# Optimization experiments

Hardware: AMD Instinct MI355X
Metric: run time of the kernel (lower is better)

Reference implementation:

```python
import jax, jax.numpy as jnp
import numpy as np

EPS = 1e-5
H = 128          # hidden_size
IN = 75          # input_size
T = 128          # seq len == window_size
B = 1024
OUT = 256        # lstm_output_size


def _bn(x, gamma, beta):
    # training-mode batch norm over the batch dim (biased variance, as in PyTorch BN)
    m = x.mean(axis=0)
    v = x.var(axis=0)
    return gamma * (x - m) * jax.lax.rsqrt(v + EPS) + beta


def _run_bnlstm_layer(xs, Wih, Whh, b, gih, bih, ghh, bhh, gc, bc):
    # xs: (T, B, D). Returns hidden stream (T, B, H).
    Bsz = xs.shape[1]
    h0 = jnp.zeros((Bsz, H), xs.dtype)
    c0 = jnp.zeros((Bsz, H), xs.dtype)

    def step(carry, x):
        h, c = carry
        gates = _bn(x @ Wih, gih, bih) + _bn(h @ Whh, ghh, bhh) + b  # (B, 4H)
        f, i, o, g = jnp.split(gates, 4, axis=1)                     # gate order f,i,o,g
        c1 = jax.nn.sigmoid(f) * c + jax.nn.sigmoid(i) * jnp.tanh(g)
        h1 = jax.nn.sigmoid(o) * jnp.tanh(_bn(c1, gc, bc))
        return (h1, c1), h1

    (_, _), hs = jax.lax.scan(step, (h0, c0), xs)
    return hs


def setup_inputs() -> dict:
    key = jax.random.key(0)
    ks = jax.random.split(key, 12)
    s = 0.05
    d = {
        'sequences': jax.random.normal(ks[0], (B, T, IN), jnp.float32),
        # layer 0 BNLSTM cell params (weights stored as (in, 4H) so y = x @ W)
        'Wih0': jax.random.normal(ks[1], (IN, 4 * H), jnp.float32) * s,
        'Whh0': jax.random.normal(ks[2], (H, 4 * H), jnp.float32) * s,
        'b0': jnp.zeros((4 * H,), jnp.float32),
        'gih0': jnp.full((4 * H,), 0.1, jnp.float32),
        'bih0': jnp.zeros((4 * H,), jnp.float32),
        'ghh0': jnp.full((4 * H,), 0.1, jnp.float32),
        'bhh0': jnp.zeros((4 * H,), jnp.float32),
        'gc0': jnp.full((H,), 0.1, jnp.float32),
        'bc0': jnp.zeros((H,), jnp.float32),
        # layer 1
        'Wih1': jax.random.normal(ks[3], (H, 4 * H), jnp.float32) * s,
        'Whh1': jax.random.normal(ks[4], (H, 4 * H), jnp.float32) * s,
        'b1': jnp.zeros((4 * H,), jnp.float32),
        'gih1': jnp.full((4 * H,), 0.1, jnp.float32),
        'bih1': jnp.zeros((4 * H,), jnp.float32),
        'ghh1': jnp.full((4 * H,), 0.1, jnp.float32),
        'bhh1': jnp.zeros((4 * H,), jnp.float32),
        'gc1': jnp.full((H,), 0.1, jnp.float32),
        'bc1': jnp.zeros((H,), jnp.float32),
        # fc: hidden -> lstm_output_size; decoder: lstm_output_size -> T*IN
        'fc_w': jax.random.normal(ks[5], (H, OUT), jnp.float32) * s,
        'fc_b': jnp.zeros((OUT,), jnp.float32),
        'dec_w': jax.random.normal(ks[6], (OUT, T * IN), jnp.float32) * s,
        'dec_b': jnp.zeros((T * IN,), jnp.float32),
    }
    return d


def reference(sequences, Wih0, Whh0, b0, gih0, bih0, ghh0, bhh0, gc0, bc0,
              Wih1, Whh1, b1, gih1, bih1, ghh1, bhh1, gc1, bc1,
              fc_w, fc_b, dec_w, dec_b):
    xs = jnp.transpose(sequences, (1, 0, 2))  # (T, B, IN), time-major
    hs0 = _run_bnlstm_layer(xs, Wih0, Whh0, b0, gih0, bih0, ghh0, bhh0, gc0, bc0)
    hs1 = _run_bnlstm_layer(hs0, Wih1, Whh1, b1, gih1, bih1, ghh1, bhh1, gc1, bc1)
    last = hs1[-1]                       # (B, H): last time step of top layer
    emb = last @ fc_w + fc_b             # (B, OUT)
    out = emb @ dec_w + dec_b            # (B, T*IN)
    return out.reshape(-1, T, IN)
```

## Files before the change

kernel.cpp:

```cpp
#include <hip/hip_runtime.h>
#include <stdint.h>
#include <stddef.h>

#define TT   128
#define BB   1024
#define INN  75
#define HH   128
#define KXP  96
#define OUTN 256
#define DECN 9600
#define EPSB 1e-5f
#define NRB  16
#define RWS  64

typedef short v8s __attribute__((ext_vector_type(8)));
typedef float v4f __attribute__((ext_vector_type(4)));
typedef unsigned short ush;
typedef unsigned int   u32;
typedef unsigned long long u64;

#define MFMA(A,B,C) __builtin_amdgcn_mfma_f32_16x16x32_bf16((A),(B),(C),0,0,0)

__device__ __align__(256) ush g_xpad[(size_t)TT * BB * KXP];
__device__ __align__(256) u64 g_G1[(size_t)TT * 32 * BB * 4];
__device__ __align__(256) ush g_wtih0[512 * KXP];
__device__ __align__(256) ush g_wthh0[512 * HH];
__device__ __align__(256) ush g_wtih1[512 * HH];
__device__ __align__(256) ush g_wthh1[512 * HH];
__device__ __align__(256) ush g_fcwt[OUTN * HH];
__device__ __align__(256) ush g_decwt[(size_t)DECN * OUTN];
__device__ __align__(256) ush g_emb[BB * OUTN];
__device__ __align__(256) u64 g_hfin[BB * 32];

__device__ __align__(256) u64 g_th0[(size_t)TT * BB * 64];
__device__ __align__(256) u64 g_gp[(size_t)2 * TT * 2 * NRB * 512];
__device__ __align__(256) u64 g_cp[(size_t)2 * TT * 2 * NRB * 64];
__device__ __align__(256) u64 g_soc[(size_t)2 * TT * 2 * BB * 64];
__device__ u32 g_ep[64];

__device__ __forceinline__ ush f2bf(float f) {
  u32 u = __float_as_uint(f);
  u32 r = (u + 0x7FFFu + ((u >> 16) & 1u)) >> 16;
  return (ush)r;
}
__device__ __forceinline__ float bf2f(ush u) { return __uint_as_float(((u32)u) << 16); }
__device__ __forceinline__ float sigf(float x)  { return 1.f / (1.f + __expf(-x)); }
__device__ __forceinline__ float tanhf_(float x){ float e = __expf(2.f * x); return 1.f - 2.f / (e + 1.f); }
__device__ __forceinline__ v8s ld8(const ush* p) { return *reinterpret_cast<const v8s*>(p); }
__device__ __forceinline__ int origcol(int m) { return (m & 3) * 128 + (m >> 4) * 4 + ((m >> 2) & 3); }

__device__ __forceinline__ u64 ald(const u64* p) {
  return __hip_atomic_load(p, __ATOMIC_RELAXED, __HIP_MEMORY_SCOPE_AGENT);
}
__device__ __forceinline__ void ast(u64* p, u64 v) {
  __hip_atomic_store(p, v, __ATOMIC_RELAXED, __HIP_MEMORY_SCOPE_AGENT);
}
__device__ __forceinline__ u64 pk24(u32 tag, float a, float b) {
  return ((u64)(tag & 0xFFFFu) << 48)
       | ((u64)(__float_as_uint(a) >> 8) << 24)
       | (u64)(__float_as_uint(b) >> 8);
}
__device__ __forceinline__ float upA24(u64 w) { return __uint_as_float(((u32)(w >> 24) & 0xFFFFFFu) << 8); }
__device__ __forceinline__ float upB24(u64 w) { return __uint_as_float(((u32)w & 0xFFFFFFu) << 8); }
__device__ __forceinline__ u32 tg16(u64 w) { return (u32)(w >> 48); }
__device__ __forceinline__ int hswz(int r, int b) { return (r * 256 + b) ^ ((r & 7) << 4); }
__device__ __forceinline__ v8s ld8l(const char* lds, int r, int b) {
  return *reinterpret_cast<const v8s*>(lds + hswz(r, b));
}

__global__ void kpackx(const float* __restrict__ seq) {
  int idx = blockIdx.x * 256 + threadIdx.x;
  int kk = idx % KXP; int rest = idx / KXP;
  int b = rest % BB;  int t = rest / BB;
  float v = (kk < INN) ? seq[((size_t)b * TT + t) * INN + kk] : 0.f;
  g_xpad[idx] = f2bf(v);
}

__global__ void kpackw(const float* __restrict__ Wih0, const float* __restrict__ Whh0,
                       const float* __restrict__ Wih1, const float* __restrict__ Whh1,
                       const float* __restrict__ fcw,  const float* __restrict__ decw) {
  int idx = blockIdx.x * 256 + threadIdx.x;
  if (idx < 49152) {
    int m = idx / KXP, k = idx % KXP;
    g_wtih0[idx] = f2bf((k < INN) ? Wih0[k * 512 + origcol(m)] : 0.f);
  } else if (idx < 114688) {
    int j = idx - 49152; int m = j / HH, k = j % HH;
    g_wthh0[j] = f2bf(Whh0[k * 512 + origcol(m)]);
  } else if (idx < 180224) {
    int j = idx - 114688; int m = j / HH, k = j % HH;
    g_wtih1[j] = f2bf(Wih1[k * 512 + origcol(m)]);
  } else if (idx < 245760) {
    int j = idx - 180224; int m = j / HH, k = j % HH;
    g_wthh1[j] = f2bf(Whh1[k * 512 + origcol(m)]);
  } else if (idx < 278528) {
    int j = idx - 245760; int c = j / HH, k = j % HH;
    g_fcwt[j] = f2bf(fcw[k * OUTN + c]);
  } else {
    int j = idx - 278528; int n = j % DECN, k = j / DECN;
    g_decwt[(size_t)n * OUTN + k] = f2bf(decw[(size_t)k * DECN + n]);
  }
}

__global__ __launch_bounds__(512) void kprep(const float* __restrict__ gih0,
                                             const float* __restrict__ bih0,
                                             const float* __restrict__ b0) {
  const int t = blockIdx.x >> 3, ct = blockIdx.x & 7;
  const int tid = threadIdx.x, wv = tid >> 6, l = tid & 63;
  const int lm = l & 15, lq = l >> 4;
  const int R0 = wv * 128;
  __shared__ float sred[8][64][2];
  __shared__ float scoef[64][2];

  v8s af[4][3];
#pragma unroll
  for (int tt = 0; tt < 4; ++tt)
#pragma unroll
    for (int ks = 0; ks < 3; ++ks)
      af[tt][ks] = ld8(&g_wtih0[(ct * 64 + tt * 16 + lm) * KXP + ks * 32 + lq * 8]);

  const v4f vz = {0.f, 0.f, 0.f, 0.f};
  v4f acc[8][4];
#pragma unroll
  for (int mt = 0; mt < 8; ++mt)
#pragma unroll
    for (int tt = 0; tt < 4; ++tt) acc[mt][tt] = vz;

#pragma unroll
  for (int mt = 0; mt < 8; ++mt) {
    const ush* xr = g_xpad + ((size_t)t * BB + R0 + mt * 16 + lm) * KXP + lq * 8;
    v8s bx0 = ld8(xr), bx1 = ld8(xr + 32), bx2 = ld8(xr + 64);
#pragma unroll
    for (int tt = 0; tt < 4; ++tt) {
      acc[mt][tt] = MFMA(af[tt][0], bx0, acc[mt][tt]);
      acc[mt][tt] = MFMA(af[tt][1], bx1, acc[mt][tt]);
      acc[mt][tt] = MFMA(af[tt][2], bx2, acc[mt][tt]);
    }
  }
  float S[4][4], Q[4][4];
#pragma unroll
  for (int tt = 0; tt < 4; ++tt)
#pragma unroll
    for (int r = 0; r < 4; ++r) {
      float s = 0.f, q = 0.f;
#pragma unroll
      for (int mt = 0; mt < 8; ++mt) { float a = acc[mt][tt][r]; s += a; q += a * a; }
#pragma unroll
      for (int off = 1; off < 16; off <<= 1) { s += __shfl_xor(s, off); q += __shfl_xor(q, off); }
      S[tt][r] = s; Q[tt][r] = q;
    }
  if (lm == 0)
#pragma unroll
    for (int tt = 0; tt < 4; ++tt)
#pragma unroll
      for (int r = 0; r < 4; ++r) {
        sred[wv][tt * 16 + lq * 4 + r][0] = S[tt][r];
        sred[wv][tt * 16 + lq * 4 + r][1] = Q[tt][r];
      }
  __syncthreads();
  if (tid < 64) {
    float Sa = 0.f, Qa = 0.f;
#pragma unroll
    for (int w8 = 0; w8 < 8; ++w8) { Sa += sred[w8][tid][0]; Qa += sred[w8][tid][1]; }
    int oc = origcol(ct * 64 + tid);
    float m_ = Sa * (1.f / BB), v_ = Qa * (1.f / BB) - m_ * m_;
    float A = gih0[oc] * rsqrtf(v_ + EPSB);
    scoef[tid][0] = A; scoef[tid][1] = bih0[oc] - A * m_ + b0[oc];
  }
  __syncthreads();
  float CA[4][4], CD[4][4];
#pragma unroll
  for (int tt = 0; tt < 4; ++tt)
#pragma unroll
    for (int r = 0; r < 4; ++r) {
      CA[tt][r] = scoef[tt * 16 + lq * 4 + r][0];
      CD[tt][r] = scoef[tt * 16 + lq * 4 + r][1];
    }
#pragma unroll
  for (int mt = 0; mt < 8; ++mt) {
    const int row = R0 + mt * 16 + lm;
#pragma unroll
    for (int tt = 0; tt < 4; ++tt) {
      const int g = ct * 4 + tt;
      u32 lo = (u32)f2bf(CA[tt][0] * acc[mt][tt][0] + CD[tt][0])
             | ((u32)f2bf(CA[tt][1] * acc[mt][tt][1] + CD[tt][1]) << 16);
      u32 hi = (u32)f2bf(CA[tt][2] * acc[mt][tt][2] + CD[tt][2])
             | ((u32)f2bf(CA[tt][3] * acc[mt][tt][3] + CD[tt][3]) << 16);
      g_G1[(((size_t)t * 32 + g) * BB + row) * 4 + lq] = (u64)lo | ((u64)hi << 32);
    }
  }
}

__global__ __launch_bounds__(512, 1) void krec7(
    const float* __restrict__ ghh0, const float* __restrict__ bhh0,
    const float* __restrict__ gc0,  const float* __restrict__ bc0,
    const float* __restrict__ gih1, const float* __restrict__ bih1,
    const float* __restrict__ ghh1, const float* __restrict__ bhh1,
    const float* __restrict__ b1,   const float* __restrict__ gc1,
    const float* __restrict__ bc1) {
  const int bid = blockIdx.x;
  const int L = bid >> 5, H = (bid >> 4) & 1, rb = bid & 15;
  const int tid = threadIdx.x, w = tid >> 6, l = tid & 63;
  const int lm = l & 15, lq = l >> 4;
  const int R0 = rb * RWS;

  __shared__ u64 s_hA_[2048];
  __shared__ u64 s_hB_[2048];
  __shared__ float s_gA[256], s_gB[256], s_bs[256];
  __shared__ float s_cgM[128], s_cbM[128];
  __shared__ float s_cA[256], s_cB[256], s_cD[256], s_mual[2][256];
  __shared__ float s_ccA[128], s_ccD[128];
  __shared__ u32 s_base;
  char* const hA = reinterpret_cast<char*>(s_hA_);
  char* const hB = reinterpret_cast<char*>(s_hB_);

  if (tid == 0)
    s_base = __hip_atomic_load(&g_ep[bid], __ATOMIC_RELAXED, __HIP_MEMORY_SCOPE_AGENT);
  if (tid < 256) {
    const int oc = origcol(H * 256 + tid);
    if (L == 0) { s_gA[tid] = ghh0[oc]; s_gB[tid] = 0.f; s_bs[tid] = bhh0[oc]; }
    else { s_gA[tid] = gih1[oc]; s_gB[tid] = ghh1[oc];
           s_bs[tid] = bih1[oc] + bhh1[oc] + b1[oc]; }
  }
  if (tid < 128) {
    s_cgM[tid] = (L ? gc1 : gc0)[tid];
    s_cbM[tid] = (L ? bc1 : bc0)[tid];
  }
  __syncthreads();
  const u32 base = s_base;

  v8s afA[2][4], afB[2][4];
  {
    const ush* wA = L ? g_wtih1 : g_wthh0;
#pragma unroll
    for (int ct = 0; ct < 2; ++ct)
#pragma unroll
      for (int ks = 0; ks < 4; ++ks) {
        const int mrow = H * 256 + (w * 2 + ct) * 16 + lm;
        afA[ct][ks] = ld8(&wA[mrow * HH + ks * 32 + lq * 8]);
        if (L) afB[ct][ks] = ld8(&g_wthh1[mrow * HH + ks * 32 + lq * 8]);
      }
  }

  float creg[4][2] = {{0.f,0.f},{0.f,0.f},{0.f,0.f},{0.f,0.f}};
  const v4f vz = {0.f, 0.f, 0.f, 0.f};

#pragma unroll 1
  for (int t = 0; t < TT; ++t) {
    const u32 tagF = base + (u32)t + 1;
    const u32 t16 = tagF & 0xFFFFu;
    v4f PA[4][2], PB[4][2];
#pragma unroll
    for (int mt = 0; mt < 4; ++mt) {
      PA[mt][0] = vz; PA[mt][1] = vz; PB[mt][0] = vz; PB[mt][1] = vz;
    }
    u64 g1v[4][2];

    if (L == 0) {
#pragma unroll
      for (int mt = 0; mt < 4; ++mt)
#pragma unroll
        for (int ct = 0; ct < 2; ++ct)
          g1v[mt][ct] = g_G1[(((size_t)t * 32 + H * 16 + w * 2 + ct) * BB
                              + R0 + mt * 16 + lm) * 4 + lq];
    } else {
      const int row = tid >> 3, j0 = (tid & 7) * 8;
      const u64* p = g_th0 + ((size_t)t * BB + R0 + row) * 64 + j0;
      u64 v[8];
#pragma unroll
      for (int k = 0; k < 8; ++k) v[k] = ald(p + k);
      for (;;) {
        bool ok = true;
#pragma unroll
        for (int k = 0; k < 8; ++k)
          if ((u32)(v[k] >> 32) != tagF) { v[k] = ald(p + k); ok = false; }
        if (ok) break;
        __builtin_amdgcn_s_sleep(1);
      }
#pragma unroll
      for (int k = 0; k < 8; ++k)
        *reinterpret_cast<u32*>(hA + hswz(row, (j0 + k) * 4)) = (u32)v[k];
    }
    __syncthreads();

    if (L == 0) {
      if (t > 0) {
#pragma unroll
        for (int mt = 0; mt < 4; ++mt)
#pragma unroll
          for (int ks = 0; ks < 4; ++ks) {
            const v8s f = ld8l(hA, mt * 16 + lm, ks * 64 + lq * 16);
            PA[mt][0] = MFMA(afA[0][ks], f, PA[mt][0]);
            PA[mt][1] = MFMA(afA[1][ks], f, PA[mt][1]);
          }
      }
    } else {
#pragma unroll
      for (int mt = 0; mt < 4; ++mt)
#pragma unroll
        for (int ks = 0; ks < 4; ++ks) {
          const v8s f = ld8l(hA, mt * 16 + lm, ks * 64 + lq * 16);
          PA[mt][0] = MFMA(afA[0][ks], f, PA[mt][0]);
          PA[mt][1] = MFMA(afA[1][ks], f, PA[mt][1]);
        }
      if (t > 0) {
#pragma unroll
        for (int mt = 0; mt < 4; ++mt)
#pragma unroll
          for (int ks = 0; ks < 4; ++ks) {
            const v8s f = ld8l(hB, mt * 16 + lm, ks * 64 + lq * 16);
            PB[mt][0] = MFMA(afB[0][ks], f, PB[mt][0]);
            PB[mt][1] = MFMA(afB[1][ks], f, PB[mt][1]);
          }
      }
    }

    u64* const gpO = g_gp + ((((size_t)L * TT + t) * 2 + H) * NRB + rb) * 512;
#pragma unroll
    for (int ct = 0; ct < 2; ++ct) {
      float sA[4], qA[4], sB[4], qB[4];
#pragma unroll
      for (int r = 0; r < 4; ++r) {
        float s1 = PA[0][ct][r] + PA[1][ct][r] + PA[2][ct][r] + PA[3][ct][r];
        float q1 = PA[0][ct][r]*PA[0][ct][r] + PA[1][ct][r]*PA[1][ct][r]
                 + PA[2][ct][r]*PA[2][ct][r] + PA[3][ct][r]*PA[3][ct][r];
        float s2 = PB[0][ct][r] + PB[1][ct][r] + PB[2][ct][r] + PB[3][ct][r];
        float q2 = PB[0][ct][r]*PB[0][ct][r] + PB[1][ct][r]*PB[1][ct][r]
                 + PB[2][ct][r]*PB[2][ct][r] + PB[3][ct][r]*PB[3][ct][r];
#pragma unroll
        for (int off = 1; off < 16; off <<= 1) {
          s1 += __shfl_xor(s1, off); q1 += __shfl_xor(q1, off);
          if (L) { s2 += __shfl_xor(s2, off); q2 += __shfl_xor(q2, off); }
        }
        sA[r] = s1; qA[r] = q1; sB[r] = s2; qB[r] = q2;
      }
      if (lm == 0) {
        const int m0 = (w * 2 + ct) * 16 + lq * 4;
#pragma unroll
        for (int r = 0; r < 4; ++r) {
          ast(&gpO[(m0 + r) * 2], pk24(tagF, sA[r], qA[r]));
          if (L) ast(&gpO[(m0 + r) * 2 + 1], pk24(tagF, sB[r], qB[r]));
        }
      }
    }
    __syncthreads();

    {
      const int st = tid >> 8, m = tid & 255;
      if (st == 0 || L == 1) {
        const u64* pb = g_gp + (((size_t)L * TT + t) * 2 + H) * NRB * 512 + m * 2 + st;
        u64 v[16];
#pragma unroll
        for (int r2 = 0; r2 < 16; ++r2) v[r2] = ald(pb + (size_t)r2 * 512);
        for (;;) {
          bool ok = true;
#pragma unroll
          for (int r2 = 0; r2 < 16; ++r2)
            if (tg16(v[r2]) != t16) { v[r2] = ald(pb + (size_t)r2 * 512); ok = false; }
          if (ok) break;
          __builtin_amdgcn_s_sleep(1);
        }
        float S = 0.f, Q = 0.f;
#pragma unroll
        for (int r2 = 0; r2 < 16; ++r2) { S += upA24(v[r2]); Q += upB24(v[r2]); }
        const float mu = S * (1.f / BB), var = Q * (1.f / BB) - mu * mu;
        const float A = (st ? s_gB[m] : s_gA[m]) * rsqrtf(var + EPSB);
        if (st == 0) s_cA[m] = A; else s_cB[m] = A;
        s_mual[st][m] = A * mu;
      }
    }
    __syncthreads();
    if (tid < 256) s_cD[tid] = s_bs[tid] - s_mual[0][tid] - (L ? s_mual[1][tid] : 0.f);
    __syncthreads();

    u64* const cpO = g_cp + ((((size_t)L * TT + t) * 2 + H) * NRB + rb) * 64;
    u64* const socO = g_soc + (((size_t)L * TT + t) * 2 + H) * BB * 64;
    float soq[4][2], cq_[4][2];
#pragma unroll
    for (int ct = 0; ct < 2; ++ct) {
      const int mb = (w * 2 + ct) * 16 + lq * 4;
      const v4f cA = *reinterpret_cast<const v4f*>(&s_cA[mb]);
      const v4f cD = *reinterpret_cast<const v4f*>(&s_cD[mb]);
      const v4f cB = *reinterpret_cast<const v4f*>(&s_cB[mb]);
      const int ul = (w * 2 + ct) * 4 + lq;
      float cs = 0.f, cqs = 0.f;
#pragma unroll
      for (int mt = 0; mt < 4; ++mt) {
        float gv[4];
        if (L == 0) {
          const u64 g1 = g1v[mt][ct];
          gv[0] = bf2f((ush)g1)         + cA[0] * PA[mt][ct][0] + cD[0];
          gv[1] = bf2f((ush)(g1 >> 16)) + cA[1] * PA[mt][ct][1] + cD[1];
          gv[2] = bf2f((ush)(g1 >> 32)) + cA[2] * PA[mt][ct][2] + cD[2];
          gv[3] = bf2f((ush)(g1 >> 48)) + cA[3] * PA[mt][ct][3] + cD[3];
        } else {
#pragma unroll
          for (int r = 0; r < 4; ++r)
            gv[r] = cA[r] * PA[mt][ct][r] + cB[r] * PB[mt][ct][r] + cD[r];
        }
        const float cold = (t == 0) ? 0.f : creg[mt][ct];
        const float c1 = sigf(gv[0]) * cold + sigf(gv[1]) * tanhf_(gv[3]);
        creg[mt][ct] = c1;
        const float so = sigf(gv[2]);
        const u64 ws = pk24(tagF, so, c1);
        ast(&socO[(size_t)(R0 + mt * 16 + lm) * 64 + ul], ws);
        const float soQ = upA24(ws), cQ = upB24(ws);
        soq[mt][ct] = soQ; cq_[mt][ct] = cQ;
        cs += cQ; cqs += cQ * cQ;
      }
#pragma unroll
      for (int off = 1; off < 16; off <<= 1) { cs += __shfl_xor(cs, off); cqs += __shfl_xor(cqs, off); }
      if (lm == 0) ast(&cpO[ul], pk24(tagF, cs, cqs));
    }
    __syncthreads();

    u64 sv[8];
    if (tid < 128) {
      const int Hs = tid >> 6, us = tid & 63;
      const u64* pc = g_cp + (((size_t)L * TT + t) * 2 + Hs) * NRB * 64 + us;
      u64 v[16];
#pragma unroll
      for (int r2 = 0; r2 < 16; ++r2) v[r2] = ald(pc + (size_t)r2 * 64);
      for (;;) {
        bool ok = true;
#pragma unroll
        for (int r2 = 0; r2 < 16; ++r2)
          if (tg16(v[r2]) != t16) { v[r2] = ald(pc + (size_t)r2 * 64); ok = false; }
        if (ok) break;
        __builtin_amdgcn_s_sleep(1);
      }
      float S = 0.f, Q = 0.f;
#pragma unroll
      for (int r2 = 0; r2 < 16; ++r2) { S += upA24(v[r2]); Q += upB24(v[r2]); }
      const float mu = S * (1.f / BB), var = Q * (1.f / BB) - mu * mu;
      const float ac = s_cgM[tid] * rsqrtf(var + EPSB);
      s_ccA[tid] = ac; s_ccD[tid] = s_cbM[tid] - ac * mu;
    }
    {
      const int rloc = tid >> 3, u0 = (tid & 7) * 8;
      const u64* ps = g_soc + (((size_t)L * TT + t) * 2 + (1 - H)) * BB * 64
                    + (size_t)(R0 + rloc) * 64 + u0;
#pragma unroll
      for (int k = 0; k < 8; ++k) sv[k] = ald(ps + k);
      for (;;) {
        bool ok = true;
#pragma unroll
        for (int k = 0; k < 8; ++k)
          if (tg16(sv[k]) != t16) { sv[k] = ald(ps + k); ok = false; }
        if (ok) break;
        __builtin_amdgcn_s_sleep(1);
      }
    }
    __syncthreads();

    char* const town = L ? hB : hA;
#pragma unroll
    for (int ct = 0; ct < 2; ++ct) {
      const int ul = (w * 2 + ct) * 4 + lq;
      const int ug = H * 64 + ul;
      const float ac = s_ccA[ug], dc = s_ccD[ug];
#pragma unroll
      for (int mt = 0; mt < 4; ++mt) {
        const int rowl = mt * 16 + lm;
        const u32 v = (u32)f2bf(soq[mt][ct] * tanhf_(ac * cq_[mt][ct] + dc));
        const u32 a = v | (__shfl_xor(v, 16) << 16);
        if (lq == 0 || lq == 2) {
          const int jg = H * 32 + (w * 2 + ct) * 2 + (lq >> 1);
          *reinterpret_cast<u32*>(town + hswz(rowl, jg * 4)) = a;
          if (L == 0)
            ast(&g_th0[((size_t)t * BB + R0 + rowl) * 64 + jg], (((u64)tagF) << 32) | a);
        }
        if (L == 1 && t == TT - 1) {
          const u32 b2 = __shfl_xor(a, 32);
          if (lq == 0)
            g_hfin[(size_t)(R0 + rowl) * 32 + H * 16 + (w * 2 + ct)] = (u64)a | ((u64)b2 << 32);
        }
      }
    }
    {
      const int rloc = tid >> 3, u0 = (tid & 7) * 8;
#pragma unroll
      for (int k = 0; k < 8; ++k) {
        const int ugs = (1 - H) * 64 + u0 + k;
        const float hs = upA24(sv[k]) * tanhf_(s_ccA[ugs] * upB24(sv[k]) + s_ccD[ugs]);
        *reinterpret_cast<ush*>(town + hswz(rloc, ugs * 2)) = f2bf(hs);
      }
    }
    __syncthreads();
  }

  if (tid == 0)
    __hip_atomic_store(&g_ep[bid], base + TT, __ATOMIC_RELAXED, __HIP_MEMORY_SCOPE_AGENT);
}

__global__ __launch_bounds__(256) void kfc(const float* __restrict__ fcb) {
  const int tid = threadIdx.x, w = tid >> 6, l = tid & 63;
  const int lm = l & 15, lq = l >> 4;
  const int col = blockIdx.x * 16 + lm;
  const ush* hsrc = reinterpret_cast<const ush*>(g_hfin);
  v8s bf[4];
#pragma unroll
  for (int ks = 0; ks < 4; ++ks) bf[ks] = ld8(&g_fcwt[col * HH + ks * 32 + lq * 8]);
  const float bias = fcb[col];
  const v4f vz = {0.f, 0.f, 0.f, 0.f};
#pragma unroll
  for (int mt = 0; mt < 16; ++mt) {
    const int rowa = w * 256 + mt * 16 + lm;
    const ush* ap = hsrc + (size_t)rowa * HH + lq * 8;
    v4f acc = vz;
#pragma unroll
    for (int ks = 0; ks < 4; ++ks)
      acc = MFMA(ld8(ap + ks * 32), bf[ks], acc);
#pragma unroll
    for (int r = 0; r < 4; ++r) {
      int row = w * 256 + mt * 16 + lq * 4 + r;
      g_emb[row * OUTN + col] = f2bf(acc[r] + bias);
    }
  }
}

__global__ __launch_bounds__(256) void kdec(const float* __restrict__ decb, float* __restrict__ out) {
  const int tid = threadIdx.x, wv = tid >> 6, l = tid & 63;
  const int lm = l & 15, lq = l >> 4;
  const int c0 = blockIdx.x * 16;
  const int R0 = wv * 256;
  v8s af[8];
#pragma unroll
  for (int ks = 0; ks < 8; ++ks) af[ks] = ld8(&g_decwt[(size_t)(c0 + lm) * OUTN + ks * 32 + lq * 8]);
  float bias[4];
#pragma unroll
  for (int r = 0; r < 4; ++r) bias[r] = decb[c0 + lq * 4 + r];
  const v4f vz = {0.f, 0.f, 0.f, 0.f};
#pragma unroll
  for (int mt = 0; mt < 16; ++mt) {
    const int row = R0 + mt * 16 + lm;
    const ush* bp = g_emb + (size_t)row * OUTN + lq * 8;
    v4f acc = vz;
#pragma unroll
    for (int ks = 0; ks < 8; ++ks)
      acc = MFMA(af[ks], ld8(bp + ks * 32), acc);
    v4f o;
#pragma unroll
    for (int r = 0; r < 4; ++r) o[r] = acc[r] + bias[r];
    *reinterpret_cast<v4f*>(&out[(size_t)row * DECN + c0 + lq * 4]) = o;
  }
}

extern "C" void kernel_launch(void* const* d_in, const int* in_sizes, int n_in,
                              void* d_out, int out_size, void* d_ws, size_t ws_size,
                              hipStream_t stream) {
  const float* seq  = (const float*)d_in[0];
  const float* Wih0 = (const float*)d_in[1];
  const float* Whh0 = (const float*)d_in[2];
  const float* b0   = (const float*)d_in[3];
  const float* gih0 = (const float*)d_in[4];
  const float* bih0 = (const float*)d_in[5];
  const float* ghh0 = (const float*)d_in[6];
  const float* bhh0 = (const float*)d_in[7];
  const float* gc0  = (const float*)d_in[8];
  const float* bc0  = (const float*)d_in[9];
  const float* Wih1 = (const float*)d_in[10];
  const float* Whh1 = (const float*)d_in[11];
  const float* b1   = (const float*)d_in[12];
  const float* gih1 = (const float*)d_in[13];
  const float* bih1 = (const float*)d_in[14];
  const float* ghh1 = (const float*)d_in[15];
  const float* bhh1 = (const float*)d_in[16];
  const float* gc1  = (const float*)d_in[17];
  const float* bc1  = (const float*)d_in[18];
  const float* fcw  = (const float*)d_in[19];
  const float* fcb  = (const float*)d_in[20];
  const float* decw = (const float*)d_in[21];
  const float* decb = (const float*)d_in[22];
  float* out = (float*)d_out;
  (void)in_sizes; (void)n_in; (void)out_size; (void)d_ws; (void)ws_size;

  kpackx<<<dim3((TT * BB * KXP) / 256), dim3(256), 0, stream>>>(seq);
  kpackw<<<dim3(10688), dim3(256), 0, stream>>>(Wih0, Whh0, Wih1, Whh1, fcw, decw);
  kprep<<<dim3(TT * 8), dim3(512), 0, stream>>>(gih0, bih0, b0);
  krec7<<<dim3(64), dim3(512), 0, stream>>>(ghh0, bhh0, gc0, bc0,
                                            gih1, bih1, ghh1, bhh1, b1, gc1, bc1);
  kfc<<<dim3(16), dim3(256), 0, stream>>>(fcb);
  kdec<<<dim3(600), dim3(256), 0, stream>>>(decb, out);
}
```

Before: 3.038 ms.

## Use 4-slot ring buffers for cross-block exchange with layer-1 backpressure flags

```diff
diff --git a/kernel.cpp b/kernel.cpp
--- a/kernel.cpp
+++ b/kernel.cpp
@@ -32,10 +32,11 @@
 __device__ __align__(256) ush g_emb[BB * OUTN];
 __device__ __align__(256) u64 g_hfin[BB * 32];
 
-__device__ __align__(256) u64 g_th0[(size_t)TT * BB * 64];
-__device__ __align__(256) u64 g_gp[(size_t)2 * TT * 2 * NRB * 512];
-__device__ __align__(256) u64 g_cp[(size_t)2 * TT * 2 * NRB * 64];
-__device__ __align__(256) u64 g_soc[(size_t)2 * TT * 2 * BB * 64];
+__device__ __align__(256) u64 g_th0[4][BB * 64];
+__device__ __align__(256) u64 g_gp[2][2][4][NRB * 512];
+__device__ __align__(256) u64 g_cp[2][4][2][NRB * 64];
+__device__ __align__(256) u64 g_soc[2][4][2][BB * 64];
+__device__ u32 g_l1p[2][NRB * 32];
 __device__ u32 g_ep[64];
 
 __device__ __forceinline__ ush f2bf(float f) {
@@ -53,6 +54,12 @@
   return __hip_atomic_load(p, __ATOMIC_RELAXED, __HIP_MEMORY_SCOPE_AGENT);
 }
 __device__ __forceinline__ void ast(u64* p, u64 v) {
+  __hip_atomic_store(p, v, __ATOMIC_RELAXED, __HIP_MEMORY_SCOPE_AGENT);
+}
+__device__ __forceinline__ u32 ald32(const u32* p) {
+  return __hip_atomic_load(p, __ATOMIC_RELAXED, __HIP_MEMORY_SCOPE_AGENT);
+}
+__device__ __forceinline__ void ast32(u32* p, u32 v) {
   __hip_atomic_store(p, v, __ATOMIC_RELAXED, __HIP_MEMORY_SCOPE_AGENT);
 }
 __device__ __forceinline__ u64 pk24(u32 tag, float a, float b) {
@@ -190,7 +197,7 @@
   }
 }
 
-__global__ __launch_bounds__(512, 1) void krec7(
+__global__ __launch_bounds__(512, 1) void krec8(
     const float* __restrict__ ghh0, const float* __restrict__ bhh0,
     const float* __restrict__ gc0,  const float* __restrict__ bc0,
     const float* __restrict__ gih1, const float* __restrict__ bih1,
@@ -213,8 +220,7 @@
   char* const hA = reinterpret_cast<char*>(s_hA_);
   char* const hB = reinterpret_cast<char*>(s_hB_);
 
-  if (tid == 0)
-    s_base = __hip_atomic_load(&g_ep[bid], __ATOMIC_RELAXED, __HIP_MEMORY_SCOPE_AGENT);
+  if (tid == 0) s_base = ald32(&g_ep[bid]);
   if (tid < 256) {
     const int oc = origcol(H * 256 + tid);
     if (L == 0) { s_gA[tid] = ghh0[oc]; s_gB[tid] = 0.f; s_bs[tid] = bhh0[oc]; }
@@ -248,6 +254,7 @@
   for (int t = 0; t < TT; ++t) {
     const u32 tagF = base + (u32)t + 1;
     const u32 t16 = tagF & 0xFFFFu;
+    const int slot = t & 3;
     v4f PA[4][2], PB[4][2];
 #pragma unroll
     for (int mt = 0; mt < 4; ++mt) {
@@ -262,9 +269,13 @@
         for (int ct = 0; ct < 2; ++ct)
           g1v[mt][ct] = g_G1[(((size_t)t * 32 + H * 16 + w * 2 + ct) * BB
                               + R0 + mt * 16 + lm) * 4 + lq];
+      if (t >= 3 && tid < 2) {
+        while (ald32(&g_l1p[tid][rb * 32]) < base + (u32)t - 2)
+          __builtin_amdgcn_s_sleep(1);
+      }
     } else {
       const int row = tid >> 3, j0 = (tid & 7) * 8;
-      const u64* p = g_th0 + ((size_t)t * BB + R0 + row) * 64 + j0;
+      const u64* p = &g_th0[slot][(R0 + row) * 64 + j0];
       u64 v[8];
 #pragma unroll
       for (int k = 0; k < 8; ++k) v[k] = ald(p + k);
@@ -281,6 +292,7 @@
         *reinterpret_cast<u32*>(hA + hswz(row, (j0 + k) * 4)) = (u32)v[k];
     }
     __syncthreads();
+    if (L == 1 && tid == 0) ast32(&g_l1p[H][rb * 32], tagF);
 
     if (L == 0) {
       if (t > 0) {
@@ -314,7 +326,7 @@
       }
     }
 
-    u64* const gpO = g_gp + ((((size_t)L * TT + t) * 2 + H) * NRB + rb) * 512;
+    u64* const gpO = &g_gp[L][H][slot][rb * 512];
 #pragma unroll
     for (int ct = 0; ct < 2; ++ct) {
       float sA[4], qA[4], sB[4], qB[4];
@@ -347,7 +359,7 @@
     {
       const int st = tid >> 8, m = tid & 255;
       if (st == 0 || L == 1) {
-        const u64* pb = g_gp + (((size_t)L * TT + t) * 2 + H) * NRB * 512 + m * 2 + st;
+        const u64* pb = &g_gp[L][H][slot][0] + m * 2 + st;
         u64 v[16];
 #pragma unroll
         for (int r2 = 0; r2 < 16; ++r2) v[r2] = ald(pb + (size_t)r2 * 512);
@@ -372,8 +384,8 @@
     if (tid < 256) s_cD[tid] = s_bs[tid] - s_mual[0][tid] - (L ? s_mual[1][tid] : 0.f);
     __syncthreads();
 
-    u64* const cpO = g_cp + ((((size_t)L * TT + t) * 2 + H) * NRB + rb) * 64;
-    u64* const socO = g_soc + (((size_t)L * TT + t) * 2 + H) * BB * 64;
+    u64* const cpO = &g_cp[L][slot][H][rb * 64];
+    u64* const socO = &g_soc[L][slot][H][0];
     float soq[4][2], cq_[4][2];
 #pragma unroll
     for (int ct = 0; ct < 2; ++ct) {
@@ -416,7 +428,7 @@
     u64 sv[8];
     if (tid < 128) {
       const int Hs = tid >> 6, us = tid & 63;
-      const u64* pc = g_cp + (((size_t)L * TT + t) * 2 + Hs) * NRB * 64 + us;
+      const u64* pc = &g_cp[L][slot][Hs][us];
       u64 v[16];
 #pragma unroll
       for (int r2 = 0; r2 < 16; ++r2) v[r2] = ald(pc + (size_t)r2 * 64);
@@ -437,8 +449,7 @@
     }
     {
       const int rloc = tid >> 3, u0 = (tid & 7) * 8;
-      const u64* ps = g_soc + (((size_t)L * TT + t) * 2 + (1 - H)) * BB * 64
-                    + (size_t)(R0 + rloc) * 64 + u0;
+      const u64* ps = &g_soc[L][slot][1 - H][(size_t)(R0 + rloc) * 64 + u0];
 #pragma unroll
       for (int k = 0; k < 8; ++k) sv[k] = ald(ps + k);
       for (;;) {
@@ -467,7 +478,7 @@
           const int jg = H * 32 + (w * 2 + ct) * 2 + (lq >> 1);
           *reinterpret_cast<u32*>(town + hswz(rowl, jg * 4)) = a;
           if (L == 0)
-            ast(&g_th0[((size_t)t * BB + R0 + rowl) * 64 + jg], (((u64)tagF) << 32) | a);
+            ast(&g_th0[slot][(R0 + rowl) * 64 + jg], (((u64)tagF) << 32) | a);
         }
         if (L == 1 && t == TT - 1) {
           const u32 b2 = __shfl_xor(a, 32);
@@ -488,8 +499,7 @@
     __syncthreads();
   }
 
-  if (tid == 0)
-    __hip_atomic_store(&g_ep[bid], base + TT, __ATOMIC_RELAXED, __HIP_MEMORY_SCOPE_AGENT);
+  if (tid == 0) ast32(&g_ep[bid], base + TT);
 }
 
 __global__ __launch_bounds__(256) void kfc(const float* __restrict__ fcb) {
@@ -577,7 +587,7 @@
   kpackx<<<dim3((TT * BB * KXP) / 256), dim3(256), 0, stream>>>(seq);
   kpackw<<<dim3(10688), dim3(256), 0, stream>>>(Wih0, Whh0, Wih1, Whh1, fcw, decw);
   kprep<<<dim3(TT * 8), dim3(512), 0, stream>>>(gih0, bih0, b0);
-  krec7<<<dim3(64), dim3(512), 0, stream>>>(ghh0, bhh0, gc0, bc0,
+  krec8<<<dim3(64), dim3(512), 0, stream>>>(ghh0, bhh0, gc0, bc0,
                                             gih1, bih1, ghh1, bhh1, b1, gc1, bc1);
   kfc<<<dim3(16), dim3(256), 0, stream>>>(fcb);
   kdec<<<dim3(600), dim3(256), 0, stream>>>(decb, out);
```

Result: no change. 3.051 ms (+0.5%).
